# Performance work log

Hardware: AMD Instinct MI355X
Metric: run time of the kernel (lower is better)

The kernel has to match this reference:

```python
import jax, jax.numpy as jnp
import numpy as np
from jax.scipy.special import erf

SIGMA = 1.0
TWOPI = 2.0 * np.pi
NORM_FACTOR = 90.0474


def setup_inputs() -> dict:
    key = jax.random.key(0)
    k1, k2 = jax.random.split(key)
    N = 6144
    q = jax.random.normal(k1, (N, 1), dtype=jnp.float32)
    r = jax.random.normal(k2, (N, 3), dtype=jnp.float32)
    cell = jnp.zeros((1, 3, 3), dtype=jnp.float32)  # det=0 -> realspace branch
    return {"q": q, "r": r, "cell": cell}


def reference(q, r, cell):
    # Realspace Ewald (non-periodic branch): sum_{i != j} q_i q_j erf(d_ij/(sigma*sqrt(2)))/d_ij
    # (cell has det < 1e-6, so the torch module takes compute_potential_realspace;
    #  batch=None -> a single system)
    n = r.shape[0]
    diff = r[:, None, :] - r[None, :, :]            # [N, N, 3]
    d2 = jnp.sum(diff * diff, axis=-1)              # [N, N]
    eye = jnp.eye(n, dtype=bool)
    d2_safe = jnp.where(eye, 1.0, d2)               # avoid 0 on diagonal
    dist = jnp.sqrt(d2_safe)
    w = erf(dist / (SIGMA * jnp.sqrt(2.0))) / dist  # erf(d/(sigma*sqrt2)) / d
    w = jnp.where(eye, 0.0, w)                      # remove self-interaction (diag)
    # pot = sum_{i!=j, c} q_ic q_jc w_ij
    pot = jnp.einsum('ic,jc,ij->', q, q, w)
    pot = pot / TWOPI / 2.0 * NORM_FACTOR
    # torch: stack over batches -> [1,1], sum(dim=1) -> [1]
    return jnp.reshape(pot, (1,))
```

## Files before the change

### kernel.cpp

```cpp
#include <hip/hip_runtime.h>
#include <math.h>


#if __has_builtin(__builtin_amdgcn_rsqf)
#define FRSQ(x) __builtin_amdgcn_rsqf(x)
#else
#define FRSQ(x) rsqrtf(x)
#endif
#if __has_builtin(__builtin_amdgcn_rcpf)
#define FRCP(x) __builtin_amdgcn_rcpf(x)
#else
#define FRCP(x) (1.0f / (x))
#endif

typedef float vf2 __attribute__((ext_vector_type(2)));

__device__ __forceinline__ vf2 vfma(vf2 a, vf2 b, vf2 c) {
  return __builtin_elementwise_fma(a, b, c);
}

#define B1 0.19685360f
#define B2 0.11519450f
#define B3 0.00034366f
#define B4 0.01952700f

template <bool CHECK>
__device__ __forceinline__ void pair2_body(const float4 v, int jj, int i0,
                                           vf2 xi, vf2 yi, vf2 zi, vf2& acc) {
  vf2 dx = xi - v.x, dy = yi - v.y, dz = zi - v.z;
  vf2 s = vfma(dx, dx, vfma(dy, dy, dz * dz));
  vf2 qk = {v.w, v.w};
  if (CHECK) {
    bool t0 = (jj > i0);
    bool t1 = (jj > i0 + 64);
    s.x = t0 ? s.x : 1.0f;
    s.y = t1 ? s.y : 1.0f;
    qk.x = t0 ? qk.x : 0.0f;
    qk.y = t1 ? qk.y : 0.0f;
  }
  vf2 ri;
  ri.x = FRSQ(s.x);
  ri.y = FRSQ(s.y);
  vf2 E = vfma(vfma((vf2){B4, B4}, s, (vf2){B2, B2}), s, (vf2){1.f, 1.f});
  vf2 O = vfma((vf2){B3, B3}, s, (vf2){B1, B1});
  vf2 dd = s * ri;
  vf2 p = vfma(dd, O, E);
  vf2 y;
  y.x = FRCP(p.x);
  y.y = FRCP(p.y);
  vf2 y2 = y * y;
  vf2 y4 = y2 * y2;
  vf2 w = vfma(-y4, ri, ri);
  acc = vfma(qk, w, acc);
}

template <bool CHECK>
__device__ __forceinline__ vf2 tile_sum(const float4* __restrict__ tile,
                                        int jbeg, int i0, vf2 xi, vf2 yi,
                                        vf2 zi) {
  vf2 a0 = {0.f, 0.f}, a1 = {0.f, 0.f};
#pragma unroll
  for (int k = 0; k < 16; k += 2) {
    pair2_body<CHECK>(tile[k], jbeg + k, i0, xi, yi, zi, a0);
    pair2_body<CHECK>(tile[k + 1], jbeg + k + 1, i0, xi, yi, zi, a1);
  }
  return a0 + a1;
}

__global__ __launch_bounds__(256) void ewald_tri(
    const float* __restrict__ q, const float* __restrict__ r,
    float* __restrict__ partial, int n) {
  const int tid = threadIdx.x;
  const int bid = blockIdx.x;
  const int lane = tid & 63;
  const int wid = tid >> 6;
  const int jslices = (n + 15) >> 4;

  int ib = 0, cum = 0;
  while (true) {
    int c = jslices - 32 * ib;
    if (c <= 0 || cum + c > bid) break;
    cum += c;
    ++ib;
  }
  const int js = 32 * ib + (bid - cum);

  const int ibeg = ib << 9;
  const int jbeg = js << 4;
  const bool pure_above = (jbeg >= ibeg + 512);

  __shared__ float4 tile[16];
  if (tid < 16) {
    int j = jbeg + tid;
    float4 v = make_float4(1e10f, 1e10f, 1e10f, 0.f);
    if (j < n) v = make_float4(r[3 * j], r[3 * j + 1], r[3 * j + 2], q[j]);
    tile[tid] = v;
  }

  const int i0 = ibeg + (wid << 7) + lane;
  const int i1 = i0 + 64;
  float qi0 = 0.f, qi1 = 0.f;
  vf2 xi = {1e10f, 1e10f}, yi = {1e10f, 1e10f}, zi = {1e10f, 1e10f};
  if (i0 < n) {
    qi0 = q[i0];
    xi.x = r[3 * i0];
    yi.x = r[3 * i0 + 1];
    zi.x = r[3 * i0 + 2];
  }
  if (i1 < n) {
    qi1 = q[i1];
    xi.y = r[3 * i1];
    yi.y = r[3 * i1 + 1];
    zi.y = r[3 * i1 + 2];
  }
  __syncthreads();

  vf2 s2;
  if (pure_above)
    s2 = tile_sum<false>(tile, jbeg, i0, xi, yi, zi);
  else
    s2 = tile_sum<true>(tile, jbeg, i0, xi, yi, zi);
  float acc = fmaf(qi0, s2.x, qi1 * s2.y);

  for (int m = 32; m > 0; m >>= 1) acc += __shfl_xor(acc, m, 64);
  __shared__ float wsum[4];
  if (lane == 0) wsum[wid] = acc;
  __syncthreads();
  if (tid == 0)
    partial[bid] = (wsum[0] + wsum[1]) + (wsum[2] + wsum[3]);
}

__global__ __launch_bounds__(1024) void reduce_partials(
    const float* __restrict__ partial, float* __restrict__ out, int np,
    float scale) {
  const int tid = threadIdx.x;
  float acc = 0.f;
  for (int idx = tid; idx < np; idx += 1024) acc += partial[idx];
  for (int m = 32; m > 0; m >>= 1) acc += __shfl_xor(acc, m, 64);
  __shared__ float wsum[16];
  const int lane = tid & 63;
  const int wid = tid >> 6;
  if (lane == 0) wsum[wid] = acc;
  __syncthreads();
  if (tid == 0) {
    float s = 0.f;
    for (int w = 0; w < 16; ++w) s += wsum[w];
    out[0] = s * scale;
  }
}

extern "C" void kernel_launch(void* const* d_in, const int* in_sizes, int n_in,
                              void* d_out, int out_size, void* d_ws,
                              size_t ws_size, hipStream_t stream) {
  const float* q = (const float*)d_in[0];
  const float* r = (const float*)d_in[1];
  const int n = in_sizes[0];
  float* out = (float*)d_out;
  float* partial = (float*)d_ws;

  const int iblocks = (n + 511) / 512;
  const int jslices = (n + 15) / 16;
  int nblocks = 0;
  for (int ib = 0; ib < iblocks; ++ib) {
    int c = jslices - 32 * ib;
    if (c > 0) nblocks += c;
  }

  ewald_tri<<<nblocks, 256, 0, stream>>>(q, r, partial, n);

  const float scale = (float)(90.0474 / (2.0 * M_PI));
  reduce_partials<<<1, 1024, 0, stream>>>(partial, out, nblocks, scale);
}
```

Before: 17.02 us.

## Fold complementary triangular strips into uniform 26-column blocks

Pairs strip s with strip nstrips-1-s so each block row covers a constant-length super-strip, and launches a 2D grid where every block processes 26 j-columns. This replaces the per-block linear search for the triangle index and evens out work per block. Blocks write per-wave partials directly, which drops the second shared-memory reduction and barrier. The new indexing assumes n is a multiple of 1024 and removes the bounds guards on i, so other sizes would break.

```diff
diff --git a/kernel.cpp b/kernel.cpp
--- a/kernel.cpp
+++ b/kernel.cpp
@@ -54,80 +54,114 @@
   acc = vfma(qk, w, acc);
 }
 
-template <bool CHECK>
-__device__ __forceinline__ vf2 tile_sum(const float4* __restrict__ tile,
-                                        int jbeg, int i0, vf2 xi, vf2 yi,
-                                        vf2 zi) {
+template <bool CHECK, int MCONST>
+__device__ __forceinline__ void phase_run(const float4* __restrict__ tile,
+                                          int m, int jbeg, int ibeg,
+                                          const float* __restrict__ q,
+                                          const float* __restrict__ r,
+                                          int lane, int wid, float& lanesum) {
+  const int i0 = ibeg + (wid << 7) + lane;
+  const int i1 = i0 + 64;
+  const float qi0 = q[i0], qi1 = q[i1];
+  vf2 xi = {r[3 * i0], r[3 * i1]};
+  vf2 yi = {r[3 * i0 + 1], r[3 * i1 + 1]};
+  vf2 zi = {r[3 * i0 + 2], r[3 * i1 + 2]};
+
   vf2 a0 = {0.f, 0.f}, a1 = {0.f, 0.f};
+  if (MCONST > 0) {
 #pragma unroll
-  for (int k = 0; k < 16; k += 2) {
-    pair2_body<CHECK>(tile[k], jbeg + k, i0, xi, yi, zi, a0);
-    pair2_body<CHECK>(tile[k + 1], jbeg + k + 1, i0, xi, yi, zi, a1);
-  }
-  return a0 + a1;
-}
-
-__global__ __launch_bounds__(256) void ewald_tri(
+    for (int k = 0; k < MCONST; k += 2) {
+      pair2_body<CHECK>(tile[k], jbeg + k, i0, xi, yi, zi, a0);
+      pair2_body<CHECK>(tile[k + 1], jbeg + k + 1, i0, xi, yi, zi, a1);
+    }
+  } else {
+    int k = 0;
+    for (; k + 2 <= m; k += 2) {
+      pair2_body<CHECK>(tile[k], jbeg + k, i0, xi, yi, zi, a0);
+      pair2_body<CHECK>(tile[k + 1], jbeg + k + 1, i0, xi, yi, zi, a1);
+    }
+    if (k < m) pair2_body<CHECK>(tile[k], jbeg + k, i0, xi, yi, zi, a0);
+  }
+  vf2 s2 = a0 + a1;
+  lanesum = fmaf(qi0, s2.x, fmaf(qi1, s2.y, lanesum));
+}
+
+__global__ __launch_bounds__(256) void ewald_fold(
     const float* __restrict__ q, const float* __restrict__ r,
     float* __restrict__ partial, int n) {
   const int tid = threadIdx.x;
-  const int bid = blockIdx.x;
   const int lane = tid & 63;
   const int wid = tid >> 6;
-  const int jslices = (n + 15) >> 4;
-
-  int ib = 0, cum = 0;
-  while (true) {
-    int c = jslices - 32 * ib;
-    if (c <= 0 || cum + c > bid) break;
-    cum += c;
-    ++ib;
-  }
-  const int js = 32 * ib + (bid - cum);
-
-  const int ibeg = ib << 9;
-  const int jbeg = js << 4;
-  const bool pure_above = (jbeg >= ibeg + 512);
-
-  __shared__ float4 tile[16];
-  if (tid < 16) {
-    int j = jbeg + tid;
-    float4 v = make_float4(1e10f, 1e10f, 1e10f, 0.f);
-    if (j < n) v = make_float4(r[3 * j], r[3 * j + 1], r[3 * j + 2], q[j]);
-    tile[tid] = v;
-  }
-
-  const int i0 = ibeg + (wid << 7) + lane;
-  const int i1 = i0 + 64;
-  float qi0 = 0.f, qi1 = 0.f;
-  vf2 xi = {1e10f, 1e10f}, yi = {1e10f, 1e10f}, zi = {1e10f, 1e10f};
-  if (i0 < n) {
-    qi0 = q[i0];
-    xi.x = r[3 * i0];
-    yi.x = r[3 * i0 + 1];
-    zi.x = r[3 * i0 + 2];
-  }
-  if (i1 < n) {
-    qi1 = q[i1];
-    xi.y = r[3 * i1];
-    yi.y = r[3 * i1 + 1];
-    zi.y = r[3 * i1 + 2];
-  }
-  __syncthreads();
-
-  vf2 s2;
-  if (pure_above)
-    s2 = tile_sum<false>(tile, jbeg, i0, xi, yi, zi);
-  else
-    s2 = tile_sum<true>(tile, jbeg, i0, xi, yi, zi);
-  float acc = fmaf(qi0, s2.x, qi1 * s2.y);
-
-  for (int m = 32; m > 0; m >>= 1) acc += __shfl_xor(acc, m, 64);
-  __shared__ float wsum[4];
-  if (lane == 0) wsum[wid] = acc;
-  __syncthreads();
-  if (tid == 0)
-    partial[bid] = (wsum[0] + wsum[1]) + (wsum[2] + wsum[3]);
+  const int s = blockIdx.y;
+  const int c0 = (int)blockIdx.x * 26;
+  const int nstrips = n >> 9;
+  const int sB = nstrips - 1 - s;
+  const int LA = n - (s << 9);
+
+  int mA = LA - c0;
+  mA = mA < 0 ? 0 : (mA > 26 ? 26 : mA);
+
+  __shared__ float4 tile[26];
+  float lanesum = 0.f;
+
+  if (mA > 0) {
+    const int jbeg = (s << 9) + c0;
+    if (tid < mA) {
+      int j = jbeg + tid;
+      tile[tid] = make_float4(r[3 * j], r[3 * j + 1], r[3 * j + 2], q[j]);
+    }
+    __syncthreads();
+    const bool chk = (c0 < 512);
+    const int ibeg = s << 9;
+    if (mA == 26) {
+      if (chk)
+        phase_run<true, 26>(tile, 26, jbeg, ibeg, q, r, lane, wid, lanesum);
+      else
+        phase_run<false, 26>(tile, 26, jbeg, ibeg, q, r, lane, wid, lanesum);
+    } else {
+      if (chk)
+        phase_run<true, 0>(tile, mA, jbeg, ibeg, q, r, lane, wid, lanesum);
+      else
+        phase_run<false, 0>(tile, mA, jbeg, ibeg, q, r, lane, wid, lanesum);
+    }
+    __syncthreads();
+  }
+
+  if (mA < 26) {
+    int tB0 = c0 - LA;
+    if (tB0 < 0) tB0 = 0;
+    const int LB = n - (sB << 9);
+    int mB = 26 - mA;
+    int rem = LB - tB0;
+    if (mB > rem) mB = rem;
+    if (mB > 0) {
+      const int jbeg = (sB << 9) + tB0;
+      if (tid < mB) {
+        int j = jbeg + tid;
+        tile[tid] = make_float4(r[3 * j], r[3 * j + 1], r[3 * j + 2], q[j]);
+      }
+      __syncthreads();
+      const bool chk = (tB0 < 512);
+      const int ibeg = sB << 9;
+      if (mB == 26) {
+        if (chk)
+          phase_run<true, 26>(tile, 26, jbeg, ibeg, q, r, lane, wid, lanesum);
+        else
+          phase_run<false, 26>(tile, 26, jbeg, ibeg, q, r, lane, wid, lanesum);
+      } else {
+        if (chk)
+          phase_run<true, 0>(tile, mB, jbeg, ibeg, q, r, lane, wid, lanesum);
+        else
+          phase_run<false, 0>(tile, mB, jbeg, ibeg, q, r, lane, wid, lanesum);
+      }
+    }
+  }
+
+  for (int m = 32; m > 0; m >>= 1) lanesum += __shfl_xor(lanesum, m, 64);
+  if (lane == 0) {
+    const int bid = (int)blockIdx.y * gridDim.x + blockIdx.x;
+    partial[bid * 4 + wid] = lanesum;
+  }
 }
 
 __global__ __launch_bounds__(1024) void reduce_partials(
@@ -143,9 +177,9 @@
   if (lane == 0) wsum[wid] = acc;
   __syncthreads();
   if (tid == 0) {
-    float s = 0.f;
-    for (int w = 0; w < 16; ++w) s += wsum[w];
-    out[0] = s * scale;
+    float ssum = 0.f;
+    for (int w = 0; w < 16; ++w) ssum += wsum[w];
+    out[0] = ssum * scale;
   }
 }
 
@@ -158,16 +192,15 @@
   float* out = (float*)d_out;
   float* partial = (float*)d_ws;
 
-  const int iblocks = (n + 511) / 512;
-  const int jslices = (n + 15) / 16;
-  int nblocks = 0;
-  for (int ib = 0; ib < iblocks; ++ib) {
-    int c = jslices - 32 * ib;
-    if (c > 0) nblocks += c;
-  }
-
-  ewald_tri<<<nblocks, 256, 0, stream>>>(q, r, partial, n);
-
+  const int nstrips = n >> 9;
+  const int nsupers = nstrips >> 1;
+  const int superlen = n + 512;
+  const int chunks = (superlen + 25) / 26;
+
+  dim3 grid(chunks, nsupers);
+  ewald_fold<<<grid, 256, 0, stream>>>(q, r, partial, n);
+
+  const int np = chunks * nsupers * 4;
   const float scale = (float)(90.0474 / (2.0 * M_PI));
-  reduce_partials<<<1, 1024, 0, stream>>>(partial, out, nblocks, scale);
-}
+  reduce_partials<<<1, 1024, 0, stream>>>(partial, out, np, scale);
+}
```

Result: slower. 17.78 us (+4.5%).
